# Kernel optimization log

Hardware: AMD Instinct MI355X
Metric: run time of the kernel (lower is better)

## Reference

```python
import jax, jax.numpy as jnp
import numpy as np

E = 2048   # embed_dim
H = 16     # num_heads
D = E // H # head_dim = 128
ROPE_BASE = 10000.0


def setup_inputs() -> dict:
    key = jax.random.key(0)
    ks = jax.random.split(key, 9)
    s = 0.02
    x = jax.random.normal(ks[0], (2, 2048, E), dtype=jnp.float32)
    Wq = jax.random.normal(ks[1], (E, E), dtype=jnp.float32) * s
    bq = jax.random.normal(ks[2], (E,), dtype=jnp.float32) * s
    Wk = jax.random.normal(ks[3], (E, E), dtype=jnp.float32) * s
    bk = jax.random.normal(ks[4], (E,), dtype=jnp.float32) * s
    Wv = jax.random.normal(ks[5], (E, E), dtype=jnp.float32) * s
    bv = jax.random.normal(ks[6], (E,), dtype=jnp.float32) * s
    Wo = jax.random.normal(ks[7], (E, E), dtype=jnp.float32) * s
    bo = jax.random.normal(ks[8], (E,), dtype=jnp.float32) * s
    return {"x": x, "Wq": Wq, "bq": bq, "Wk": Wk, "bk": bk,
            "Wv": Wv, "bv": bv, "Wo": Wo, "bo": bo}


def _rope_cos_sin(seq_len, dtype):
    inv_freq = 1.0 / (ROPE_BASE ** (jnp.arange(0, D, 2, dtype=jnp.float32) / D))
    pos = jnp.arange(seq_len, dtype=jnp.float32)
    freqs = pos[:, None] * inv_freq[None, :]          # (S, D/2)
    emb = jnp.concatenate([freqs, freqs], axis=-1)    # (S, D)
    return jnp.cos(emb).astype(dtype), jnp.sin(emb).astype(dtype)


def _rotate_half(t):
    t1, t2 = jnp.split(t, 2, axis=-1)
    return jnp.concatenate([-t2, t1], axis=-1)


def reference(x, Wq, bq, Wk, bk, Wv, bv, Wo, bo):
    B, S, _ = x.shape
    # QKV projections (torch Linear: x @ W.T + b)
    q = (x @ Wq.T + bq).reshape(B, S, H, D).transpose(0, 2, 1, 3)  # (B,H,S,D)
    k = (x @ Wk.T + bk).reshape(B, S, H, D).transpose(0, 2, 1, 3)
    v = (x @ Wv.T + bv).reshape(B, S, H, D).transpose(0, 2, 1, 3)
    # RoPE
    cos, sin = _rope_cos_sin(S, x.dtype)              # (S, D) each
    q = q * cos + _rotate_half(q) * sin
    k = k * cos + _rotate_half(k) * sin
    # Causal scaled dot-product attention
    scale = 1.0 / jnp.sqrt(jnp.asarray(D, dtype=x.dtype))
    scores = jnp.einsum('bhqd,bhkd->bhqk', q, k) * scale
    causal = jnp.tril(jnp.ones((S, S), dtype=bool))
    scores = jnp.where(causal, scores, jnp.asarray(-jnp.inf, dtype=x.dtype))
    attn = jax.nn.softmax(scores, axis=-1)
    out = jnp.einsum('bhqk,bhkd->bhqd', attn, v)      # (B,H,S,D)
    out = out.transpose(0, 2, 1, 3).reshape(B, S, E)
    return out @ Wo.T + bo
```

## Files before the change

kernel.cpp:

```cpp
#include <hip/hip_runtime.h>
#include <math.h>

typedef __bf16 bf16;
typedef __attribute__((ext_vector_type(2))) __bf16 bf16x2;
typedef __attribute__((ext_vector_type(4))) __bf16 bf16x4;
typedef __attribute__((ext_vector_type(8))) __bf16 bf16x8;
typedef __attribute__((ext_vector_type(4))) float f32x4;

#define GLD16(g, l) __builtin_amdgcn_global_load_lds( \
    (const __attribute__((address_space(1))) void*)(g), \
    (__attribute__((address_space(3))) void*)(l), 16, 0, 0)

template<int N> __device__ __forceinline__ void wait_vm() {
  static_assert(N == 0 || N == 2 || N == 3, "");
  if constexpr (N == 0) asm volatile("s_waitcnt vmcnt(0)" ::: "memory");
  else if constexpr (N == 2) asm volatile("s_waitcnt vmcnt(2)" ::: "memory");
  else asm volatile("s_waitcnt vmcnt(3)" ::: "memory");
}

__global__ void prep_kernel(const float* __restrict__ x,
                            const float* __restrict__ Wq, const float* __restrict__ Wk,
                            const float* __restrict__ Wv, const float* __restrict__ Wo,
                            const float* __restrict__ bq, const float* __restrict__ bk,
                            const float* __restrict__ bv,
                            bf16* __restrict__ xb, bf16* __restrict__ wqkv, bf16* __restrict__ wob,
                            float* __restrict__ biasq, float* __restrict__ cost, float* __restrict__ sint) {
  const int bid = blockIdx.x, t = threadIdx.x;
  if (bid < 24576) {
    const float* src;
    bf16* dst;
    int i;
    if (bid < 8192)       { src = x;  dst = xb;                    i = bid * 256 + t; }
    else if (bid < 12288) { src = Wq; dst = wqkv;                  i = (bid - 8192) * 256 + t; }
    else if (bid < 16384) { src = Wk; dst = wqkv + 2048 * 2048;    i = (bid - 12288) * 256 + t; }
    else if (bid < 20480) { src = Wv; dst = wqkv + 2 * 2048 * 2048; i = (bid - 16384) * 256 + t; }
    else                  { src = Wo; dst = wob;                   i = (bid - 20480) * 256 + t; }
    float4 f = ((const float4*)src)[i];
    bf16x4 o;
    o[0] = (bf16)f.x; o[1] = (bf16)f.y; o[2] = (bf16)f.z; o[3] = (bf16)f.w;
    ((bf16x4*)dst)[i] = o;
  } else if (bid < 25088) {
    int i = (bid - 24576) * 256 + t;
    int s = i >> 6, d = i & 63;
    float inv = powf(10000.0f, -(float)d / 64.0f);
    float ang = (float)s * inv;
    cost[i] = cosf(ang);
    sint[i] = sinf(ang);
  } else {
    int i = (bid - 25088) * 256 + t;
    biasq[i] = (i < 2048) ? bq[i] : (i < 4096 ? bk[i - 2048] : bv[i - 4096]);
  }
}

__global__ void rope_tv_kernel(const bf16* __restrict__ qkv,
                               const float* __restrict__ cost, const float* __restrict__ sint,
                               bf16* __restrict__ kr, bf16* __restrict__ vt) {
  __shared__ bf16 Vl[64 * 72];
  const int t = threadIdx.x;
  if (blockIdx.x < 4096) {
    int idx = blockIdx.x * 256 + t;
    int dp = idx & 15;
    int h = (idx >> 4) & 15;
    int s = (idx >> 8) & 2047;
    int b = idx >> 19;
    int d0 = dp * 4;
    const bf16* row = qkv + ((size_t)(b * 2048 + s) * 6144) + 2048 + h * 128;
    bf16x4 klo = *(const bf16x4*)&row[d0];
    bf16x4 khi = *(const bf16x4*)&row[d0 + 64];
    float4 c4 = *(const float4*)&cost[(s << 6) + d0];
    float4 s4 = *(const float4*)&sint[(s << 6) + d0];
    float cf[4] = {c4.x, c4.y, c4.z, c4.w};
    float sf[4] = {s4.x, s4.y, s4.z, s4.w};
    bf16x4 olo, ohi;
#pragma unroll
    for (int j = 0; j < 4; ++j) {
      float kl = (float)klo[j], kh = (float)khi[j];
      olo[j] = (bf16)(kl * cf[j] - kh * sf[j]);
      ohi[j] = (bf16)(kh * cf[j] + kl * sf[j]);
    }
    bf16* orow = kr + (((size_t)(b * 16 + h) * 2048 + s) * 128);
    *(bf16x4*)&orow[d0] = olo;
    *(bf16x4*)&orow[d0 + 64] = ohi;
  } else {
    int vbid = blockIdx.x - 4096;
    const int dt = vbid & 1, st = (vbid >> 1) & 31, bh = vbid >> 6;
    const int b = bh >> 4, h = bh & 15;
    const bf16* src = qkv + ((size_t)(b * 2048 + st * 64) * 6144) + 4096 + h * 128 + dt * 64;
    bf16* dst = vt + ((size_t)bh * 128 + dt * 64) * 2048 + st * 64;
#pragma unroll
    for (int i = 0; i < 2; ++i) {
      int c = i * 256 + t;
      int r = c >> 3, c0 = (c & 7) * 8;
      *(bf16x8*)&Vl[r * 72 + c0] = *(const bf16x8*)&src[(size_t)r * 6144 + c0];
    }
    __syncthreads();
#pragma unroll
    for (int i = 0; i < 2; ++i) {
      int c = i * 256 + t;
      int r = c >> 3, c0 = (c & 7) * 8;
      bf16x8 v;
#pragma unroll
      for (int j = 0; j < 8; ++j) v[j] = Vl[(c0 + j) * 72 + r];
      *(bf16x8*)&dst[(size_t)r * 2048 + c0] = v;
    }
  }
}

template<int BN, bool OUT_BF16>
__global__ __launch_bounds__(512, 2)
void gemm256_kernel(const bf16* __restrict__ A, const bf16* __restrict__ B,
                    const float* __restrict__ bias, void* __restrict__ Cp,
                    int M, int N, int K) {
  constexpr int NB = BN / 64;
  __shared__ bf16 Al[2][2][128 * 64];
  __shared__ bf16 Bl[2][NB][64 * 64];
  const int t = threadIdx.x;
  const int wid = t >> 6, lane = t & 63;
  const int wr = wid >> 2, wc = wid & 3;
  const int lr = lane & 15, lk = lane >> 4;
  const int flat = (int)blockIdx.x;
  const int xcd = flat & 7, kb2 = flat >> 3;
  const int tm = xcd * 2 + (kb2 & 1);
  const int tn = kb2 >> 1;
  const bf16* Ab = A + (size_t)tm * 256 * K;
  const bf16* Bb = B + (size_t)tn * BN * K;
  const int NT = K >> 6;

  auto stageA = [&](int bp, int h, int kt) {
#pragma unroll
    for (int q = 0; q < 2; ++q) {
      int e = q * 512 + t;
      int r = e >> 3, c = e & 7;
      GLD16(Ab + (size_t)(h * 128 + r) * K + kt * 64 + ((c ^ (r & 7)) << 3), &Al[bp][h][e * 8]);
    }
  };
  auto stageB = [&](int bp, int unit, int kt) {
    int r = t >> 3, c = t & 7;
    GLD16(Bb + (size_t)(unit * 64 + r) * K + kt * 64 + ((c ^ (r & 7)) << 3), &Bl[bp][unit][t * 8]);
  };

  f32x4 acc[8][NB] = {};

#pragma unroll
  for (int un = 0; un < NB; ++un) stageB(0, un, 0);
  stageA(0, 0, 0); stageA(0, 1, 0);
  if (NT > 1) {
#pragma unroll
    for (int un = 0; un < NB; ++un) stageB(1, un, 1);
    wait_vm<NB>();
  } else {
    wait_vm<0>();
  }
  __builtin_amdgcn_s_barrier();
  __builtin_amdgcn_sched_barrier(0);

  for (int u = 0; u < NT; ++u) {
    const int p = u & 1;
    const bf16* Ah = Al[p][wr];
    bf16x8 bfr[NB][2];
#pragma unroll
    for (int j = 0; j < 4; ++j) {
      bf16x8 afr[2][2];
      if (j == 0) {
#pragma unroll
        for (int n = 0; n < NB; ++n)
#pragma unroll
          for (int kk = 0; kk < 2; ++kk) {
            int rb = wc * (NB * 16) + n * 16 + lr;
            bfr[n][kk] = *(const bf16x8*)&Bl[p][rb >> 6][(rb & 63) * 64 + ((((kk << 2) | lk) ^ (rb & 7)) << 3)];
          }
      }
#pragma unroll
      for (int m2 = 0; m2 < 2; ++m2)
#pragma unroll
        for (int kk = 0; kk < 2; ++kk) {
          int r = (2 * j + m2) * 16 + lr;
          afr[m2][kk] = *(const bf16x8*)&Ah[r * 64 + ((((kk << 2) | lk) ^ (r & 7)) << 3)];
        }
      if (j == 0)      { if (u + 1 < NT) stageA(p ^ 1, 0, u + 1); }
      else if (j == 1) { if (u + 1 < NT) stageA(p ^ 1, 1, u + 1); }
      else if (j == 2) {
        if (u + 2 < NT) {
#pragma unroll
          for (int un = 0; un < NB / 2; ++un) stageB(p, un, u + 2);
        }
      } else {
        if (u + 2 < NT) {
#pragma unroll
          for (int un = NB / 2; un < NB; ++un) stageB(p, un, u + 2);
        }
      }
      __builtin_amdgcn_s_barrier();
      asm volatile("s_waitcnt lgkmcnt(0)" ::: "memory");
      __builtin_amdgcn_sched_barrier(0);
      __builtin_amdgcn_s_setprio(1);
#pragma unroll
      for (int m2 = 0; m2 < 2; ++m2)
#pragma unroll
        for (int n = 0; n < NB; ++n)
#pragma unroll
          for (int kk = 0; kk < 2; ++kk)
            acc[2 * j + m2][n] = __builtin_amdgcn_mfma_f32_16x16x32_bf16(
                afr[m2][kk], bfr[n][kk], acc[2 * j + m2][n], 0, 0, 0);
      __builtin_amdgcn_s_setprio(0);
      __builtin_amdgcn_sched_barrier(0);
      if (j == 3) {
        if (u + 2 < NT) { wait_vm<NB>(); }
        else            { wait_vm<0>(); }
      }
      __builtin_amdgcn_s_barrier();
      __builtin_amdgcn_sched_barrier(0);
    }
  }

  const int rb = tm * 256 + wr * 128, cb = tn * BN + wc * (NB * 16);
#pragma unroll
  for (int n = 0; n < NB; ++n) {
    int col = cb + n * 16 + lr;
    float bvl = bias[col];
#pragma unroll
    for (int m = 0; m < 8; ++m) {
#pragma unroll
      for (int r = 0; r < 4; ++r) {
        int row = rb + m * 16 + lk * 4 + r;
        float v = acc[m][n][r] + bvl;
        if (OUT_BF16) ((bf16*)Cp)[(size_t)row * N + col] = (bf16)v;
        else          ((float*)Cp)[(size_t)row * N + col] = v;
      }
    }
  }
}

__global__ __launch_bounds__(256, 2)
void attn_kernel(const bf16* __restrict__ qkv, const bf16* __restrict__ Kc,
                 const bf16* __restrict__ Vtg, const float* __restrict__ cost,
                 const float* __restrict__ sint, bf16* __restrict__ O, int S) {
  __shared__ bf16 Kl[2][64 * 128];
  __shared__ bf16 Vt[2][128 * 64];
  __shared__ bf16 Pl[4][16 * 64];
  const int t = threadIdx.x, wid = t >> 6, lane = t & 63;
  const int lr = lane & 15, lk = lane >> 4;
  const int flat = (int)blockIdx.x;
  const int xcd = flat & 7, kk2 = flat >> 3;
  const int bh = xcd * 4 + (kk2 >> 4);
  const int b = bh >> 4, h = bh & 15;
  const int NQ = S >> 6;
  const int qtA = kk2 & 15, qtB = NQ - 1 - qtA;
  const int ntA = qtA + 1, ntB = qtB + 1, total = ntA + ntB;
  const bf16* Kb = Kc + (size_t)bh * S * 128;
  const bf16* Vb = Vtg + (size_t)bh * 128 * S;
  const float scale = 0.08838834764831845f;

  bf16x8 qf[4];
  auto loadQ = [&](int q0) {
    int qrow = q0 + wid * 16 + lr;
    const bf16* qp = qkv + (size_t)(b * 2048 + qrow) * 6144 + h * 128;
    bf16x8 raw[4];
#pragma unroll
    for (int kb = 0; kb < 4; ++kb) raw[kb] = *(const bf16x8*)&qp[kb * 32 + lk * 8];
#pragma unroll
    for (int kb = 0; kb < 4; ++kb) {
      const float* cb = cost + (qrow << 6) + ((kb & 1) << 5) + lk * 8;
      const float* sb = sint + (qrow << 6) + ((kb & 1) << 5) + lk * 8;
#pragma unroll
      for (int j = 0; j < 8; ++j) {
        float qv = (float)raw[kb][j];
        float qo = (float)raw[kb ^ 2][j];
        float rot = (kb < 2) ? -qo : qo;
        qf[kb][j] = (bf16)(qv * cb[j] + rot * sb[j]);
      }
    }
  };
  auto stage = [&](int buf, int kv0) {
#pragma unroll
    for (int c = 0; c < 4; ++c) {
      int fc = c * 256 + t;
      int kvr = fc >> 4, cc = fc & 15;
      GLD16(Kb + (size_t)(kv0 + kvr) * 128 + (cc ^ (kvr & 7)) * 8, &Kl[buf][fc * 8]);
      int dr = fc >> 3, c2 = fc & 7;
      GLD16(Vb + (size_t)dr * S + kv0 + (c2 ^ (dr & 7)) * 8, &Vt[buf][fc * 8]);
    }
  };

  f32x4 o[8] = {};
  float mrun[4], lrun[4];
#pragma unroll
  for (int r = 0; r < 4; ++r) { mrun[r] = -INFINITY; lrun[r] = 0.f; }

  loadQ(qtA * 64);
  stage(0, 0);
  __syncthreads();
  int cur = 0;
  for (int ti = 0; ti < total; ++ti) {
    if (ti + 1 < total) {
      int tn = ti + 1;
      stage(cur ^ 1, ((tn < ntA) ? tn : tn - ntA) * 64);
    }
    __builtin_amdgcn_sched_barrier(0);
    const bool isA = ti < ntA;
    const int tt = isA ? ti : ti - ntA;
    const int nt = isA ? ntA : ntB;
    const int q0 = (isA ? qtA : qtB) * 64;
    const int kv0 = tt * 64;
    f32x4 sa[4];
    __builtin_amdgcn_s_setprio(1);
#pragma unroll
    for (int n = 0; n < 4; ++n) {
      sa[n] = (f32x4){0.f, 0.f, 0.f, 0.f};
      int kvl = n * 16 + lr;
#pragma unroll
      for (int kb = 0; kb < 4; ++kb) {
        bf16x8 kf = *(const bf16x8*)&Kl[cur][kvl * 128 + (((kb << 2) | lk) ^ (kvl & 7)) * 8];
        sa[n] = __builtin_amdgcn_mfma_f32_16x16x32_bf16(qf[kb], kf, sa[n], 0, 0, 0);
      }
    }
    __builtin_amdgcn_s_setprio(0);
    float p[4][4];
    float tmax[4] = {-INFINITY, -INFINITY, -INFINITY, -INFINITY};
    const bool lastTile = (tt == nt - 1);
#pragma unroll
    for (int n = 0; n < 4; ++n)
#pragma unroll
      for (int r = 0; r < 4; ++r) {
        float s = sa[n][r] * scale;
        if (lastTile) {
          int kvg = kv0 + n * 16 + lr;
          int qg = q0 + wid * 16 + lk * 4 + r;
          if (kvg > qg) s = -INFINITY;
        }
        p[n][r] = s;
        tmax[r] = fmaxf(tmax[r], s);
      }
#pragma unroll
    for (int r = 0; r < 4; ++r)
#pragma unroll
      for (int off = 1; off < 16; off <<= 1)
        tmax[r] = fmaxf(tmax[r], __shfl_xor(tmax[r], off));
    float alpha[4], rsum[4];
#pragma unroll
    for (int r = 0; r < 4; ++r) {
      float mnew = fmaxf(mrun[r], tmax[r]);
      alpha[r] = __expf(mrun[r] - mnew);
      mrun[r] = mnew;
      rsum[r] = 0.f;
#pragma unroll
      for (int n = 0; n < 4; ++n) {
        p[n][r] = __expf(p[n][r] - mnew);
        rsum[r] += p[n][r];
      }
    }
#pragma unroll
    for (int r = 0; r < 4; ++r) {
#pragma unroll
      for (int off = 1; off < 16; off <<= 1)
        rsum[r] += __shfl_xor(rsum[r], off);
      lrun[r] = lrun[r] * alpha[r] + rsum[r];
    }
#pragma unroll
    for (int n8 = 0; n8 < 8; ++n8)
#pragma unroll
      for (int r = 0; r < 4; ++r)
        o[n8][r] *= alpha[r];
#pragma unroll
    for (int n = 0; n < 4; ++n)
#pragma unroll
      for (int r = 0; r < 4; ++r) {
        int row = lk * 4 + r, col = n * 16 + lr;
        Pl[wid][(row * 64 + col) ^ ((row & 7) << 3)] = (bf16)p[n][r];
      }
    __builtin_amdgcn_s_setprio(1);
#pragma unroll
    for (int kb2 = 0; kb2 < 2; ++kb2) {
      bf16x8 pf = *(const bf16x8*)&Pl[wid][(lr * 64 + kb2 * 32 + lk * 8) ^ ((lr & 7) << 3)];
#pragma unroll
      for (int n8 = 0; n8 < 8; ++n8) {
        int dcol = n8 * 16 + lr;
        bf16x8 vf = *(const bf16x8*)&Vt[cur][(dcol * 64 + kb2 * 32 + lk * 8) ^ ((dcol & 7) << 3)];
        o[n8] = __builtin_amdgcn_mfma_f32_16x16x32_bf16(pf, vf, o[n8], 0, 0, 0);
      }
    }
    __builtin_amdgcn_s_setprio(0);
    if (ti == ntA - 1) {
#pragma unroll
      for (int r = 0; r < 4; ++r) {
        float rl = 1.0f / lrun[r];
        int row = qtA * 64 + wid * 16 + lk * 4 + r;
        size_t base = ((size_t)(b * S + row)) * 2048 + h * 128;
#pragma unroll
        for (int n8 = 0; n8 < 8; ++n8)
          O[base + n8 * 16 + lr] = (bf16)(o[n8][r] * rl);
      }
#pragma unroll
      for (int n8 = 0; n8 < 8; ++n8) o[n8] = (f32x4){0.f, 0.f, 0.f, 0.f};
#pragma unroll
      for (int r = 0; r < 4; ++r) { mrun[r] = -INFINITY; lrun[r] = 0.f; }
      loadQ(qtB * 64);
    }
    __syncthreads();
    cur ^= 1;
  }
#pragma unroll
  for (int r = 0; r < 4; ++r) {
    float rl = 1.0f / lrun[r];
    int row = qtB * 64 + wid * 16 + lk * 4 + r;
    size_t base = ((size_t)(b * S + row)) * 2048 + h * 128;
#pragma unroll
    for (int n8 = 0; n8 < 8; ++n8)
      O[base + n8 * 16 + lr] = (bf16)(o[n8][r] * rl);
  }
}


extern "C" void kernel_launch(void* const* d_in, const int* in_sizes, int n_in,
                              void* d_out, int out_size, void* d_ws, size_t ws_size,
                              hipStream_t stream) {
  const float* x  = (const float*)d_in[0];
  const float* Wq = (const float*)d_in[1];
  const float* bq = (const float*)d_in[2];
  const float* Wk = (const float*)d_in[3];
  const float* bk = (const float*)d_in[4];
  const float* Wv = (const float*)d_in[5];
  const float* bv = (const float*)d_in[6];
  const float* Wo = (const float*)d_in[7];
  const float* bo = (const float*)d_in[8];

  char* ws = (char*)d_ws;
  bf16* xb     = (bf16*)(ws);
  bf16* wqkv   = (bf16*)(ws + 16777216);
  bf16* wob    = (bf16*)(ws + 41943040);
  bf16* qkv    = (bf16*)(ws + 50331648);
  bf16* kr     = (bf16*)(ws + 100663296);
  bf16* vt     = (bf16*)(ws + 117440512);
  float* biasq = (float*)(ws + 134217728);
  float* cost  = (float*)(ws + 134242304);
  float* sint  = (float*)(ws + 134766592);
  bf16* attn_out = xb;

  prep_kernel<<<25112, 256, 0, stream>>>(x, Wq, Wk, Wv, Wo, bq, bk, bv,
                                         xb, wqkv, wob, biasq, cost, sint);
  gemm256_kernel<192, true><<<512, 512, 0, stream>>>(xb, wqkv, biasq, qkv, 4096, 6144, 2048);
  rope_tv_kernel<<<6144, 256, 0, stream>>>(qkv, cost, sint, kr, vt);
  attn_kernel<<<512, 256, 0, stream>>>(qkv, kr, vt, cost, sint, attn_out, 2048);
  gemm256_kernel<128, false><<<256, 512, 0, stream>>>(attn_out, wob, bo, (float*)d_out, 4096, 2048, 2048);
}
```

Measured before the change: 289.5 us.

## Shrink GEMM tiles to 128-row blocks with four waves, raise attention occupancy

Both projection GEMMs move from 256-row, 8-wave (512-thread) blocks to 128-row, 4-wave (256-thread) blocks, doubling the grid size. Per-thread staging loads and vmcnt waits are adjusted to match, and the XCD tile mapping changes. The smaller tiles should give more blocks per device and better load balance across CUs, at the cost of less reuse per tile and more global traffic. Separately, attn_kernel's launch bounds are raised to 3 blocks per CU, which caps register use to allow more occupancy.

```diff
diff --git a/kernel.cpp b/kernel.cpp
--- a/kernel.cpp
+++ b/kernel.cpp
@@ -12,10 +12,10 @@
     (__attribute__((address_space(3))) void*)(l), 16, 0, 0)
 
 template<int N> __device__ __forceinline__ void wait_vm() {
-  static_assert(N == 0 || N == 2 || N == 3, "");
+  static_assert(N == 0 || N == 4 || N == 6, "");
   if constexpr (N == 0) asm volatile("s_waitcnt vmcnt(0)" ::: "memory");
-  else if constexpr (N == 2) asm volatile("s_waitcnt vmcnt(2)" ::: "memory");
-  else asm volatile("s_waitcnt vmcnt(3)" ::: "memory");
+  else if constexpr (N == 4) asm volatile("s_waitcnt vmcnt(4)" ::: "memory");
+  else asm volatile("s_waitcnt vmcnt(6)" ::: "memory");
 }
 
 __global__ void prep_kernel(const float* __restrict__ x,
@@ -107,39 +107,46 @@
 }
 
 template<int BN, bool OUT_BF16>
-__global__ __launch_bounds__(512, 2)
-void gemm256_kernel(const bf16* __restrict__ A, const bf16* __restrict__ B,
-                    const float* __restrict__ bias, void* __restrict__ Cp,
-                    int M, int N, int K) {
+__global__ __launch_bounds__(256, 2)
+void gemm4w_kernel(const bf16* __restrict__ A, const bf16* __restrict__ B,
+                   const float* __restrict__ bias, void* __restrict__ Cp,
+                   int M, int N, int K) {
   constexpr int NB = BN / 64;
-  __shared__ bf16 Al[2][2][128 * 64];
+  constexpr int NR = BN / 32;
+  __shared__ bf16 Al[2][128 * 64];
   __shared__ bf16 Bl[2][NB][64 * 64];
   const int t = threadIdx.x;
   const int wid = t >> 6, lane = t & 63;
-  const int wr = wid >> 2, wc = wid & 3;
+  const int wr = wid >> 1, wc = wid & 1;
   const int lr = lane & 15, lk = lane >> 4;
   const int flat = (int)blockIdx.x;
-  const int xcd = flat & 7, kb2 = flat >> 3;
-  const int tm = xcd * 2 + (kb2 & 1);
-  const int tn = kb2 >> 1;
-  const bf16* Ab = A + (size_t)tm * 256 * K;
+  const int xcd = flat & 7, r0 = flat >> 3;
+  const int tm = xcd * 4 + (r0 & 3);
+  const int tn = r0 >> 2;
+  const bf16* Ab = A + (size_t)tm * 128 * K;
   const bf16* Bb = B + (size_t)tn * BN * K;
   const int NT = K >> 6;
 
   auto stageA = [&](int bp, int h, int kt) {
 #pragma unroll
     for (int q = 0; q < 2; ++q) {
-      int e = q * 512 + t;
+      int e = q * 256 + t;
       int r = e >> 3, c = e & 7;
-      GLD16(Ab + (size_t)(h * 128 + r) * K + kt * 64 + ((c ^ (r & 7)) << 3), &Al[bp][h][e * 8]);
+      GLD16(Ab + (size_t)(h * 64 + r) * K + kt * 64 + ((c ^ (r & 7)) << 3),
+            &Al[bp][h * 4096 + e * 8]);
     }
   };
   auto stageB = [&](int bp, int unit, int kt) {
-    int r = t >> 3, c = t & 7;
-    GLD16(Bb + (size_t)(unit * 64 + r) * K + kt * 64 + ((c ^ (r & 7)) << 3), &Bl[bp][unit][t * 8]);
+#pragma unroll
+    for (int q = 0; q < 2; ++q) {
+      int e = q * 256 + t;
+      int r = e >> 3, c = e & 7;
+      GLD16(Bb + (size_t)(unit * 64 + r) * K + kt * 64 + ((c ^ (r & 7)) << 3),
+            &Bl[bp][unit][e * 8]);
+    }
   };
 
-  f32x4 acc[8][NB] = {};
+  f32x4 acc[4][NR] = {};
 
 #pragma unroll
   for (int un = 0; un < NB; ++un) stageB(0, un, 0);
@@ -147,7 +154,7 @@
   if (NT > 1) {
 #pragma unroll
     for (int un = 0; un < NB; ++un) stageB(1, un, 1);
-    wait_vm<NB>();
+    wait_vm<2 * NB>();
   } else {
     wait_vm<0>();
   }
@@ -156,56 +163,48 @@
 
   for (int u = 0; u < NT; ++u) {
     const int p = u & 1;
-    const bf16* Ah = Al[p][wr];
-    bf16x8 bfr[NB][2];
+    bf16x8 bfr[NR][2];
 #pragma unroll
     for (int j = 0; j < 4; ++j) {
-      bf16x8 afr[2][2];
       if (j == 0) {
 #pragma unroll
-        for (int n = 0; n < NB; ++n)
+        for (int n = 0; n < NR; ++n)
 #pragma unroll
           for (int kk = 0; kk < 2; ++kk) {
-            int rb = wc * (NB * 16) + n * 16 + lr;
+            int rb = wc * (NR * 16) + n * 16 + lr;
             bfr[n][kk] = *(const bf16x8*)&Bl[p][rb >> 6][(rb & 63) * 64 + ((((kk << 2) | lk) ^ (rb & 7)) << 3)];
           }
       }
-#pragma unroll
-      for (int m2 = 0; m2 < 2; ++m2)
-#pragma unroll
-        for (int kk = 0; kk < 2; ++kk) {
-          int r = (2 * j + m2) * 16 + lr;
-          afr[m2][kk] = *(const bf16x8*)&Ah[r * 64 + ((((kk << 2) | lk) ^ (r & 7)) << 3)];
-        }
+      bf16x8 afr[2];
+      {
+        int row = wr * 64 + j * 16 + lr;
+#pragma unroll
+        for (int kk = 0; kk < 2; ++kk)
+          afr[kk] = *(const bf16x8*)&Al[p][row * 64 + ((((kk << 2) | lk) ^ (row & 7)) << 3)];
+      }
       if (j == 0)      { if (u + 1 < NT) stageA(p ^ 1, 0, u + 1); }
       else if (j == 1) { if (u + 1 < NT) stageA(p ^ 1, 1, u + 1); }
       else if (j == 2) {
         if (u + 2 < NT) {
 #pragma unroll
-          for (int un = 0; un < NB / 2; ++un) stageB(p, un, u + 2);
+          for (int un = 0; un < NB - 1; ++un) stageB(p, un, u + 2);
         }
       } else {
-        if (u + 2 < NT) {
-#pragma unroll
-          for (int un = NB / 2; un < NB; ++un) stageB(p, un, u + 2);
-        }
+        if (u + 2 < NT) stageB(p, NB - 1, u + 2);
       }
       __builtin_amdgcn_s_barrier();
       asm volatile("s_waitcnt lgkmcnt(0)" ::: "memory");
       __builtin_amdgcn_sched_barrier(0);
       __builtin_amdgcn_s_setprio(1);
 #pragma unroll
-      for (int m2 = 0; m2 < 2; ++m2)
-#pragma unroll
-        for (int n = 0; n < NB; ++n)
-#pragma unroll
-          for (int kk = 0; kk < 2; ++kk)
-            acc[2 * j + m2][n] = __builtin_amdgcn_mfma_f32_16x16x32_bf16(
-                afr[m2][kk], bfr[n][kk], acc[2 * j + m2][n], 0, 0, 0);
+      for (int n = 0; n < NR; ++n)
+#pragma unroll
+        for (int kk = 0; kk < 2; ++kk)
+          acc[j][n] = __builtin_amdgcn_mfma_f32_16x16x32_bf16(afr[kk], bfr[n][kk], acc[j][n], 0, 0, 0);
       __builtin_amdgcn_s_setprio(0);
       __builtin_amdgcn_sched_barrier(0);
       if (j == 3) {
-        if (u + 2 < NT) { wait_vm<NB>(); }
+        if (u + 2 < NT) { wait_vm<2 * NB>(); }
         else            { wait_vm<0>(); }
       }
       __builtin_amdgcn_s_barrier();
@@ -213,17 +212,17 @@
     }
   }
 
-  const int rb = tm * 256 + wr * 128, cb = tn * BN + wc * (NB * 16);
-#pragma unroll
-  for (int n = 0; n < NB; ++n) {
-    int col = cb + n * 16 + lr;
+  const int rbase = tm * 128 + wr * 64, cbase = tn * BN + wc * (NR * 16);
+#pragma unroll
+  for (int n = 0; n < NR; ++n) {
+    int col = cbase + n * 16 + lr;
     float bvl = bias[col];
 #pragma unroll
-    for (int m = 0; m < 8; ++m) {
-#pragma unroll
-      for (int r = 0; r < 4; ++r) {
-        int row = rb + m * 16 + lk * 4 + r;
-        float v = acc[m][n][r] + bvl;
+    for (int m = 0; m < 4; ++m) {
+#pragma unroll
+      for (int rr = 0; rr < 4; ++rr) {
+        int row = rbase + m * 16 + lk * 4 + rr;
+        float v = acc[m][n][rr] + bvl;
         if (OUT_BF16) ((bf16*)Cp)[(size_t)row * N + col] = (bf16)v;
         else          ((float*)Cp)[(size_t)row * N + col] = v;
       }
@@ -231,7 +230,7 @@
   }
 }
 
-__global__ __launch_bounds__(256, 2)
+__global__ __launch_bounds__(256, 3)
 void attn_kernel(const bf16* __restrict__ qkv, const bf16* __restrict__ Kc,
                  const bf16* __restrict__ Vtg, const float* __restrict__ cost,
                  const float* __restrict__ sint, bf16* __restrict__ O, int S) {
@@ -438,8 +437,8 @@
 
   prep_kernel<<<25112, 256, 0, stream>>>(x, Wq, Wk, Wv, Wo, bq, bk, bv,
                                          xb, wqkv, wob, biasq, cost, sint);
-  gemm256_kernel<192, true><<<512, 512, 0, stream>>>(xb, wqkv, biasq, qkv, 4096, 6144, 2048);
+  gemm4w_kernel<192, true><<<1024, 256, 0, stream>>>(xb, wqkv, biasq, qkv, 4096, 6144, 2048);
   rope_tv_kernel<<<6144, 256, 0, stream>>>(qkv, cost, sint, kr, vt);
   attn_kernel<<<512, 256, 0, stream>>>(qkv, kr, vt, cost, sint, attn_out, 2048);
-  gemm256_kernel<128, false><<<256, 512, 0, stream>>>(attn_out, wob, bo, (float*)d_out, 4096, 2048, 2048);
-}
+  gemm4w_kernel<128, false><<<512, 256, 0, stream>>>(attn_out, wob, bo, (float*)d_out, 4096, 2048, 2048);
+}
```

After: 287.4 us. No clear change (-0.7%).
